# Performance work log

Measured on AMD Instinct MI355X. Metric: run time of the kernel, lower is better.

The kernel has to match this reference:

```python
import jax, jax.numpy as jnp
import numpy as np

N_CTX = 4096
D_MODEL = 1024
D_HEAD = 64


def setup_inputs() -> dict:
    key = jax.random.key(0)
    k_x, k_q, k_k, k_o, k_v = jax.random.split(key, 5)
    return {
        "x": jax.random.normal(k_x, (N_CTX, D_MODEL), dtype=jnp.float32),
        "W_q": jax.random.normal(k_q, (D_MODEL, D_HEAD), dtype=jnp.float32),
        "W_kT": jax.random.normal(k_k, (D_HEAD, D_MODEL), dtype=jnp.float32),
        "W_o": jax.random.normal(k_o, (D_MODEL, D_HEAD), dtype=jnp.float32),
        "W_vT": jax.random.normal(k_v, (D_HEAD, D_MODEL), dtype=jnp.float32),
    }


def reference(x, W_q, W_kT, W_o, W_vT):
    # x: [n, d_model]
    n = x.shape[0]
    q = x @ W_q                      # [n, d_head]
    k = x @ W_kT.T                   # [n, d_head]  (W_kT @ x.T transposed)
    scores = q @ k.T                 # [n, n] -- NOTE: original has no 1/sqrt(d_head) scaling
    # causal mask: upper triangle (strictly above diagonal) set to -inf
    causal = jnp.tril(jnp.ones((n, n), dtype=bool))
    scores = jnp.where(causal, scores, -jnp.inf)
    attn = jax.nn.softmax(scores, axis=1)  # softmax over keys (dim=1)
    v = x @ W_o @ W_vT               # [n, d_model] -- faithful to attn @ x @ W_o @ W_vT
    return attn @ v                  # [n, d_model]
```

## Files before the change

kernel.cpp:

```cpp
#include <hip/hip_runtime.h>
#include <hip/hip_bf16.h>
#include <math.h>

#define DM    1024
#define DH    64
#define NCTX  4096
#define NCH   8

typedef __attribute__((ext_vector_type(8))) short bf16x8;
typedef __attribute__((ext_vector_type(4))) float f32x4;

#define D_QH   0
#define D_QM   524288
#define D_QL   1048576
#define D_KH   1572864
#define D_KM   2097152
#define D_KL   2621440
#define D_UTB  3145728
#define D_PY   3670016
#define D_PM   12058624
#define D_PL   12189696
#define D_WTH  12320768
#define D_WTM  12713984

#define S_WVH  0
#define S_WVM  131072
#define S_PM   262144
#define S_PL   393216
#define S_PY   524288
#define S_END  8912896
#define S_YH   262144
#define S_YM   786432

__device__ __forceinline__ ushort f2bf(float x) {
  __hip_bfloat16 h = __float2bfloat16(x);
  return __builtin_bit_cast(ushort, h);
}
__device__ __forceinline__ float bf2f(ushort u) {
  __hip_bfloat16 h = __builtin_bit_cast(__hip_bfloat16, u);
  return __bfloat162float(h);
}

typedef __attribute__((address_space(1))) const unsigned int gas_u32;
typedef __attribute__((address_space(3))) unsigned int las_u32;
__device__ __forceinline__ void gload_lds16(const void* g, void* l) {
  __builtin_amdgcn_global_load_lds((gas_u32*)g, (las_u32*)l, 16, 0, 0);
}

__global__ __launch_bounds__(256) void wsplit_kernel(
    const float* __restrict__ Wq, const float* __restrict__ WkT,
    const float* __restrict__ Wo, const float* __restrict__ Wv,
    ushort* __restrict__ WTh, ushort* __restrict__ WTm,
    ushort* __restrict__ WvTh, ushort* __restrict__ WvTm)
{
  int gid = blockIdx.x * 256 + threadIdx.x;
  int mat = gid >> 16;
  int idx = gid & 65535;
  if (mat == 3) {
    float v = Wv[idx];
    int h = idx >> 10, c = idx & 1023;
    int oidx = c * 64 + h;
    ushort h16 = f2bf(v);
    WvTh[oidx] = h16;
    WvTm[oidx] = f2bf(v - bf2f(h16));
    return;
  }
  float v; int oidx;
  if (mat == 1) {
    v = WkT[idx];
    oidx = 65536 + idx;
  } else {
    int k = idx >> 6, h = idx & 63;
    v = (mat == 0 ? Wq : Wo)[idx];
    oidx = mat * 65536 + h * 1024 + k;
  }
  ushort h16 = f2bf(v);
  float rem = v - bf2f(h16);
  WTh[oidx] = h16;
  WTm[oidx] = f2bf(rem);
}

__global__ __launch_bounds__(256, 2) void proj_mfma_kernel(
    const float* __restrict__ x,
    const ushort* __restrict__ WTh, const ushort* __restrict__ WTm,
    ushort* __restrict__ Qh, ushort* __restrict__ Qm, ushort* __restrict__ Ql,
    ushort* __restrict__ Kh, ushort* __restrict__ Km, ushort* __restrict__ Kl,
    ushort* __restrict__ UTb)
{
  __shared__ __align__(16) ushort xsh[32*128], xsm[32*128];
  __shared__ __align__(16) ushort wsh[2][64*128], wsm[2][64*128];

  const int tid  = threadIdx.x;
  const int lane = tid & 63;
  const int w    = tid >> 6;
  const int q16  = lane & 15;
  const int grp  = lane >> 4;
  const int r0   = blockIdx.x * 32;
  const int mat  = blockIdx.y;
  const ushort* __restrict__ wh = WTh + mat * 65536;
  const ushort* __restrict__ wm = WTm + mat * 65536;

  const int rw  = (w & 1) * 16;
  const int ct0 = (w >> 1) * 2;

  const int xrowl = tid >> 4, xslot = tid & 15;

  auto stage_w = [&](int b, int s) {
    const int kp0 = s * 128;
    #pragma unroll
    for (int u = 0; u < 4; ++u) {
      int ubase = u * 256 + w * 64;
      int unit  = ubase + lane;
      int row   = unit >> 4, slotp = unit & 15;
      int ssrc  = slotp ^ (row & 15);
      int gsrc  = row * DM + kp0 + ssrc * 8;
      gload_lds16(&wh[gsrc], &wsh[b][ubase * 8]);
      gload_lds16(&wm[gsrc], &wsm[b][ubase * 8]);
    }
  };
  auto xload = [&](int s, float4& a0, float4& a1, float4& b0, float4& b1) {
    const int kp0 = s * 128;
    const float* s0 = &x[(r0 + xrowl) * DM + kp0 + xslot * 8];
    const float* s1 = &x[(r0 + xrowl + 16) * DM + kp0 + xslot * 8];
    a0 = *(const float4*)&s0[0]; a1 = *(const float4*)&s0[4];
    b0 = *(const float4*)&s1[0]; b1 = *(const float4*)&s1[4];
  };
  auto xsplit_write = [&](float4 a0, float4 a1, float4 b0, float4 b1) {
    float xv0[8] = {a0.x,a0.y,a0.z,a0.w,a1.x,a1.y,a1.z,a1.w};
    float xv1[8] = {b0.x,b0.y,b0.z,b0.w,b1.x,b1.y,b1.z,b1.w};
    bf16x8 hv0, mv0, hv1, mv1;
    #pragma unroll
    for (int e = 0; e < 8; ++e) {
      ushort h0 = f2bf(xv0[e]);
      hv0[e] = (short)h0;  mv0[e] = (short)f2bf(xv0[e] - bf2f(h0));
      ushort h1 = f2bf(xv1[e]);
      hv1[e] = (short)h1;  mv1[e] = (short)f2bf(xv1[e] - bf2f(h1));
    }
    int d0 = xrowl * 128 + ((xslot ^ (xrowl & 15)) << 3);
    int r1 = xrowl + 16;
    int d1 = r1 * 128 + ((xslot ^ (r1 & 15)) << 3);
    *(bf16x8*)&xsh[d0] = hv0;  *(bf16x8*)&xsm[d0] = mv0;
    *(bf16x8*)&xsh[d1] = hv1;  *(bf16x8*)&xsm[d1] = mv1;
  };

  f32x4 acc[2] = {{0,0,0,0},{0,0,0,0}};

  {
    float4 a0, a1, b0, b1;
    xload(0, a0, a1, b0, b1);
    xsplit_write(a0, a1, b0, b1);
    stage_w(0, 0);
  }
  __syncthreads();

  int cur = 0;
  for (int stg = 0; stg < 8; ++stg) {
    float4 na0, na1, nb0, nb1;
    if (stg < 7) {
      xload(stg + 1, na0, na1, nb0, nb1);
      stage_w(cur ^ 1, stg + 1);
    }
    #pragma unroll
    for (int ksub = 0; ksub < 4; ++ksub) {
      const int s = ksub * 4 + grp;
      const int xrow = rw + q16;
      bf16x8 xh8 = *(const bf16x8*)&xsh[xrow * 128 + ((s ^ (xrow & 15)) << 3)];
      bf16x8 xm8 = *(const bf16x8*)&xsm[xrow * 128 + ((s ^ (xrow & 15)) << 3)];
      #pragma unroll
      for (int i = 0; i < 2; ++i) {
        const int wrow = (ct0 + i) * 16 + q16;
        const int woff = wrow * 128 + ((s ^ (wrow & 15)) << 3);
        bf16x8 bh = *(const bf16x8*)&wsh[cur][woff];
        bf16x8 bm = *(const bf16x8*)&wsm[cur][woff];
        if (mat == 2) {
          acc[i] = __builtin_amdgcn_mfma_f32_16x16x32_bf16(bh, xh8, acc[i], 0,0,0);
          acc[i] = __builtin_amdgcn_mfma_f32_16x16x32_bf16(bh, xm8, acc[i], 0,0,0);
          acc[i] = __builtin_amdgcn_mfma_f32_16x16x32_bf16(bm, xh8, acc[i], 0,0,0);
          acc[i] = __builtin_amdgcn_mfma_f32_16x16x32_bf16(bm, xm8, acc[i], 0,0,0);
        } else {
          acc[i] = __builtin_amdgcn_mfma_f32_16x16x32_bf16(xh8, bh, acc[i], 0,0,0);
          acc[i] = __builtin_amdgcn_mfma_f32_16x16x32_bf16(xh8, bm, acc[i], 0,0,0);
          acc[i] = __builtin_amdgcn_mfma_f32_16x16x32_bf16(xm8, bh, acc[i], 0,0,0);
          acc[i] = __builtin_amdgcn_mfma_f32_16x16x32_bf16(xm8, bm, acc[i], 0,0,0);
        }
      }
    }
    __syncthreads();
    if (stg < 7) xsplit_write(na0, na1, nb0, nb1);
    __syncthreads();
    cur ^= 1;
  }

  if (mat == 2) {
    #pragma unroll
    for (int i = 0; i < 2; ++i)
      #pragma unroll
      for (int r = 0; r < 4; ++r)
        UTb[((ct0 + i)*16 + 4*grp + r) * NCTX + r0 + rw + q16] = f2bf(acc[i][r]);
  } else {
    ushort* __restrict__ Dh = (mat == 0) ? Qh : Kh;
    ushort* __restrict__ Dm = (mat == 0) ? Qm : Km;
    ushort* __restrict__ Dl = (mat == 0) ? Ql : Kl;
    #pragma unroll
    for (int i = 0; i < 2; ++i)
      #pragma unroll
      for (int r = 0; r < 4; ++r) {
        float v = acc[i][r];
        ushort h = f2bf(v); float fh = bf2f(h);
        ushort m = f2bf(v - fh); float fm = bf2f(m);
        ushort l = f2bf(v - fh - fm);
        int idx = (r0 + rw + 4*grp + r) * DH + (ct0 + i)*16 + q16;
        Dh[idx] = h; Dm[idx] = m; Dl[idx] = l;
      }
  }
}

__global__ __launch_bounds__(256, 2) void attn_kernel(
    const ushort* __restrict__ Qh, const ushort* __restrict__ Qm, const ushort* __restrict__ Ql,
    const ushort* __restrict__ Kh, const ushort* __restrict__ Km, const ushort* __restrict__ Kl,
    const ushort* __restrict__ UTb,
    float* __restrict__ Pm, float* __restrict__ Pl, float* __restrict__ Py)
{
  __shared__ ushort Ksh[2][3][64*64];
  __shared__ ushort Ush[2][64*64];
  __shared__ __align__(16) ushort ps[4][16*72];

  const int tid  = threadIdx.x;
  const int lane = tid & 63;
  const int w    = tid >> 6;
  ushort* psw = ps[w];
  const int q16  = lane & 15;
  const int grp  = lane >> 4;
  const int colb = grp * 8;

  const int qq    = blockIdx.x;
  const int c     = blockIdx.y;
  const int gbase = 252 - 4 * qq;
  const int g     = gbase + w;
  const int gmax  = gbase + 3;
  const int T     = ((16*gmax + 15) >> 6) + 1;
  const int t0 = (c * T) >> 3, t1 = ((c+1) * T) >> 3;
  const int Town = ((16*g + 15) >> 6) + 1;
  const int q0 = 16 * g;
  const int q  = q0 + q16;

  auto stage = [&](int b, int t) {
    const int j0 = t * 64;
    #pragma unroll
    for (int it = 0; it < 2; ++it) {
      int ubase = it * 256 + w * 64;
      int unit  = ubase + lane;
      int row   = unit >> 3, slotp = unit & 7;
      int c8    = slotp ^ (row & 7);
      int src   = (j0 + row) * DH + c8 * 8;
      gload_lds16(&Kh[src], &Ksh[b][0][ubase * 8]);
      gload_lds16(&Km[src], &Ksh[b][1][ubase * 8]);
      gload_lds16(&Kl[src], &Ksh[b][2][ubase * 8]);
      gload_lds16(&UTb[row * NCTX + j0 + c8 * 8], &Ush[b][ubase * 8]);
    }
  };

  bf16x8 fqh[2], fqm[2], fql[2];
  #pragma unroll
  for (int ks = 0; ks < 2; ++ks) {
    int off = (q0 + q16)*DH + 32*ks + colb;
    fqh[ks] = *(const bf16x8*)&Qh[off];
    fqm[ks] = *(const bf16x8*)&Qm[off];
    fql[ks] = *(const bf16x8*)&Ql[off];
  }

  float mrun = -3.0e38f, lrun = 0.f;
  f32x4 yacc[4] = {{0,0,0,0},{0,0,0,0},{0,0,0,0},{0,0,0,0}};

  if (t0 < t1) stage(0, t0);
  __syncthreads();

  int cur = 0;
  for (int t = t0; t < t1; ++t) {
    if (t + 1 < t1) stage(cur ^ 1, t + 1);
    if (t < Town) {
      const int j0 = t * 64;
      f32x4 sa[4] = {{0,0,0,0},{0,0,0,0},{0,0,0,0},{0,0,0,0}};
      #pragma unroll
      for (int ks = 0; ks < 2; ++ks) {
        #pragma unroll
        for (int st = 0; st < 4; ++st) {
          int row = 16*st + q16;
          int off = row * 64 + (((4*ks + grp) ^ (row & 7)) << 3);
          bf16x8 kh = *(const bf16x8*)&Ksh[cur][0][off];
          bf16x8 km = *(const bf16x8*)&Ksh[cur][1][off];
          bf16x8 kl = *(const bf16x8*)&Ksh[cur][2][off];
          sa[st] = __builtin_amdgcn_mfma_f32_16x16x32_bf16(kh, fqh[ks], sa[st], 0,0,0);
          sa[st] = __builtin_amdgcn_mfma_f32_16x16x32_bf16(kh, fqm[ks], sa[st], 0,0,0);
          sa[st] = __builtin_amdgcn_mfma_f32_16x16x32_bf16(km, fqh[ks], sa[st], 0,0,0);
          sa[st] = __builtin_amdgcn_mfma_f32_16x16x32_bf16(km, fqm[ks], sa[st], 0,0,0);
          sa[st] = __builtin_amdgcn_mfma_f32_16x16x32_bf16(kh, fql[ks], sa[st], 0,0,0);
          sa[st] = __builtin_amdgcn_mfma_f32_16x16x32_bf16(kl, fqh[ks], sa[st], 0,0,0);
        }
      }
      #pragma unroll
      for (int st = 0; st < 4; ++st)
        #pragma unroll
        for (int r = 0; r < 4; ++r) {
          int key = j0 + 16*st + 4*grp + r;
          if (key > q) sa[st][r] = -3.0e38f;
        }
      float mx = sa[0][0];
      #pragma unroll
      for (int st = 0; st < 4; ++st)
        #pragma unroll
        for (int r = 0; r < 4; ++r) mx = fmaxf(mx, sa[st][r]);
      mx = fmaxf(mx, __shfl_xor(mx, 16));
      mx = fmaxf(mx, __shfl_xor(mx, 32));
      float mnew  = fmaxf(mrun, mx);
      float alpha = __expf(mrun - mnew);
      float ts = 0.f;
      ushort pb[16];
      #pragma unroll
      for (int st = 0; st < 4; ++st)
        #pragma unroll
        for (int r = 0; r < 4; ++r) {
          float p = __expf(sa[st][r] - mnew);
          ts += p;
          pb[st*4 + r] = f2bf(p);
        }
      ts += __shfl_xor(ts, 16);
      ts += __shfl_xor(ts, 32);
      lrun = lrun * alpha + ts;
      mrun = mnew;
      float ar[4];
      #pragma unroll
      for (int r = 0; r < 4; ++r) ar[r] = __shfl(alpha, 4*grp + r, 64);
      #pragma unroll
      for (int dt = 0; dt < 4; ++dt) {
        yacc[dt][0] *= ar[0]; yacc[dt][1] *= ar[1];
        yacc[dt][2] *= ar[2]; yacc[dt][3] *= ar[3];
      }
      #pragma unroll
      for (int st = 0; st < 4; ++st) {
        uint2 v;
        v.x = (uint)pb[st*4+0] | ((uint)pb[st*4+1] << 16);
        v.y = (uint)pb[st*4+2] | ((uint)pb[st*4+3] << 16);
        *(uint2*)&psw[q16*72 + 16*st + 4*grp] = v;
      }
      __threadfence_block();
      __builtin_amdgcn_sched_barrier(0);
      #pragma unroll
      for (int ks = 0; ks < 2; ++ks) {
        bf16x8 pa = *(const bf16x8*)&psw[q16*72 + 32*ks + colb];
        #pragma unroll
        for (int dt = 0; dt < 4; ++dt) {
          int row = 16*dt + q16;
          int off = row * 64 + (((4*ks + grp) ^ (row & 7)) << 3);
          bf16x8 ub = *(const bf16x8*)&Ush[cur][off];
          yacc[dt] = __builtin_amdgcn_mfma_f32_16x16x32_bf16(pa, ub, yacc[dt], 0,0,0);
        }
      }
    }
    __syncthreads();
    cur ^= 1;
  }
  if (grp == 0) {
    Pm[c * NCTX + q] = mrun;
    Pl[c * NCTX + q] = lrun;
  }
  #pragma unroll
  for (int dt = 0; dt < 4; ++dt)
    #pragma unroll
    for (int r = 0; r < 4; ++r)
      Py[(c * NCTX + q0 + 4*grp + r) * DH + 16*dt + q16] = yacc[dt][r];
}

__global__ __launch_bounds__(256, 3) void out_fused_kernel(
    const float* __restrict__ Pm, const float* __restrict__ Pl,
    const float* __restrict__ Py,
    const ushort* __restrict__ WvTh, const ushort* __restrict__ WvTm,
    float* __restrict__ out)
{
  __shared__ __align__(16) ushort Yh[64*64], Ym[64*64];
  __shared__ __align__(16) ushort Wsh[128*64], Wsm[128*64];
  __shared__ float sden[NCH][64];
  __shared__ float invd[64];

  const int tid  = threadIdx.x;
  const int lane = tid & 63;
  const int w    = tid >> 6;
  const int q16  = lane & 15;
  const int grp  = lane >> 4;
  const int r0   = blockIdx.x * 64;
  const int cb   = blockIdx.y;

  #pragma unroll
  for (int u = 0; u < 4; ++u) {
    int ubase = u * 256 + w * 64;
    int unit  = ubase + lane;
    int row   = unit >> 3, slotp = unit & 7;
    int c8    = slotp ^ (row & 7);
    int src   = (cb * 128 + row) * 64 + c8 * 8;
    gload_lds16(&WvTh[src], &Wsh[ubase * 8]);
    gload_lds16(&WvTm[src], &Wsm[ubase * 8]);
  }
  if (tid < 64) {
    int rrow = r0 + tid;
    float mv[NCH]; float M = -3.0e38f;
    #pragma unroll
    for (int c = 0; c < NCH; ++c) {
      mv[c] = Pm[c*NCTX + rrow];
      M = fmaxf(M, mv[c]);
    }
    float den = 0.f;
    #pragma unroll
    for (int c = 0; c < NCH; ++c) {
      float s = __expf(mv[c] - M);
      sden[c][tid] = s;
      den += s * Pl[c*NCTX + rrow];
    }
    invd[tid] = 1.0f / den;
  }
  __syncthreads();

  #pragma unroll
  for (int it = 0; it < 4; ++it) {
    int idx = it * 256 + tid;
    int h4 = idx & 15, rr = idx >> 4;
    int rrow = r0 + rr;
    float nx = 0.f, ny = 0.f, nz = 0.f, nw = 0.f;
    #pragma unroll
    for (int c = 0; c < NCH; ++c) {
      float s = sden[c][rr];
      float4 p4 = *(const float4*)&Py[(c*NCTX + rrow)*DH + h4*4];
      nx += s*p4.x; ny += s*p4.y; nz += s*p4.z; nw += s*p4.w;
    }
    float inv = invd[rr];
    float yv[4] = {nx*inv, ny*inv, nz*inv, nw*inv};
    ushort hv[4], mv4[4];
    #pragma unroll
    for (int e = 0; e < 4; ++e) {
      ushort h = f2bf(yv[e]);
      hv[e] = h;
      mv4[e] = f2bf(yv[e] - bf2f(h));
    }
    int off = rr*64 + (((h4 >> 1) ^ (rr & 7)) << 3) + (h4 & 1) * 4;
    uint2 vh, vm;
    vh.x = (uint)hv[0] | ((uint)hv[1] << 16);
    vh.y = (uint)hv[2] | ((uint)hv[3] << 16);
    vm.x = (uint)mv4[0] | ((uint)mv4[1] << 16);
    vm.y = (uint)mv4[2] | ((uint)mv4[3] << 16);
    *(uint2*)&Yh[off] = vh;
    *(uint2*)&Ym[off] = vm;
  }
  __syncthreads();

  f32x4 acc[4][2] = {};
  #pragma unroll
  for (int ks = 0; ks < 2; ++ks) {
    bf16x8 ah[4], am[4];
    #pragma unroll
    for (int rt = 0; rt < 4; ++rt) {
      int row = 16*rt + q16;
      int off = row*64 + (((4*ks + grp) ^ (row & 7)) << 3);
      ah[rt] = *(const bf16x8*)&Yh[off];
      am[rt] = *(const bf16x8*)&Ym[off];
    }
    #pragma unroll
    for (int lt = 0; lt < 2; ++lt) {
      int crow = w*32 + lt*16 + q16;
      int off  = crow*64 + (((4*ks + grp) ^ (crow & 7)) << 3);
      bf16x8 bh = *(const bf16x8*)&Wsh[off];
      bf16x8 bm = *(const bf16x8*)&Wsm[off];
      #pragma unroll
      for (int rt = 0; rt < 4; ++rt) {
        acc[rt][lt] = __builtin_amdgcn_mfma_f32_16x16x32_bf16(ah[rt], bh, acc[rt][lt], 0,0,0);
        acc[rt][lt] = __builtin_amdgcn_mfma_f32_16x16x32_bf16(ah[rt], bm, acc[rt][lt], 0,0,0);
        acc[rt][lt] = __builtin_amdgcn_mfma_f32_16x16x32_bf16(am[rt], bh, acc[rt][lt], 0,0,0);
        acc[rt][lt] = __builtin_amdgcn_mfma_f32_16x16x32_bf16(am[rt], bm, acc[rt][lt], 0,0,0);
      }
    }
  }
  #pragma unroll
  for (int rt = 0; rt < 4; ++rt)
    #pragma unroll
    for (int lt = 0; lt < 2; ++lt)
      #pragma unroll
      for (int r = 0; r < 4; ++r)
        out[(r0 + 16*rt + 4*grp + r) * DM + cb*128 + w*32 + lt*16 + q16] = acc[rt][lt][r];
}

__global__ __launch_bounds__(256) void combine_kernel(
    const float* __restrict__ Pm, const float* __restrict__ Pl,
    const float* __restrict__ Py,
    ushort* __restrict__ Yh, ushort* __restrict__ Ym)
{
  int idx = blockIdx.x * 256 + threadIdx.x;
  int r = idx >> 6, d = idx & 63;
  float mv[NCH];
  float M = -3.0e38f;
  #pragma unroll
  for (int c = 0; c < NCH; ++c) {
    mv[c] = Pm[c*NCTX + r];
    M = fmaxf(M, mv[c]);
  }
  float num = 0.f, den = 0.f;
  #pragma unroll
  for (int c = 0; c < NCH; ++c) {
    float s = __expf(mv[c] - M);
    den += s * Pl[c*NCTX + r];
    num += s * Py[(c*NCTX + r)*DH + d];
  }
  float y = num / den;
  ushort h = f2bf(y);
  Yh[idx] = h;
  Ym[idx] = f2bf(y - bf2f(h));
}

__global__ __launch_bounds__(256, 3) void out_mfma_kernel(
    const ushort* __restrict__ Yh_g, const ushort* __restrict__ Ym_g,
    const ushort* __restrict__ WvTh, const ushort* __restrict__ WvTm,
    float* __restrict__ out)
{
  __shared__ __align__(16) ushort Yh[64*64], Ym[64*64];
  __shared__ __align__(16) ushort Wsh[128*64], Wsm[128*64];

  const int tid  = threadIdx.x;
  const int lane = tid & 63;
  const int w    = tid >> 6;
  const int q16  = lane & 15;
  const int grp  = lane >> 4;
  const int r0   = blockIdx.x * 64;
  const int cb   = blockIdx.y;

  #pragma unroll
  for (int it = 0; it < 2; ++it) {
    int ubase = it * 256 + w * 64;
    int unit  = ubase + lane;
    int row   = unit >> 3, slotp = unit & 7;
    int c8    = slotp ^ (row & 7);
    int src   = (r0 + row) * 64 + c8 * 8;
    gload_lds16(&Yh_g[src], &Yh[ubase * 8]);
    gload_lds16(&Ym_g[src], &Ym[ubase * 8]);
  }
  #pragma unroll
  for (int u = 0; u < 4; ++u) {
    int ubase = u * 256 + w * 64;
    int unit  = ubase + lane;
    int row   = unit >> 3, slotp = unit & 7;
    int c8    = slotp ^ (row & 7);
    int src   = (cb * 128 + row) * 64 + c8 * 8;
    gload_lds16(&WvTh[src], &Wsh[ubase * 8]);
    gload_lds16(&WvTm[src], &Wsm[ubase * 8]);
  }
  __syncthreads();

  f32x4 acc[4][2] = {};
  #pragma unroll
  for (int ks = 0; ks < 2; ++ks) {
    bf16x8 ah[4], am[4];
    #pragma unroll
    for (int rt = 0; rt < 4; ++rt) {
      int row = 16*rt + q16;
      int off = row*64 + (((4*ks + grp) ^ (row & 7)) << 3);
      ah[rt] = *(const bf16x8*)&Yh[off];
      am[rt] = *(const bf16x8*)&Ym[off];
    }
    #pragma unroll
    for (int lt = 0; lt < 2; ++lt) {
      int crow = w*32 + lt*16 + q16;
      int off  = crow*64 + (((4*ks + grp) ^ (crow & 7)) << 3);
      bf16x8 bh = *(const bf16x8*)&Wsh[off];
      bf16x8 bm = *(const bf16x8*)&Wsm[off];
      #pragma unroll
      for (int rt = 0; rt < 4; ++rt) {
        acc[rt][lt] = __builtin_amdgcn_mfma_f32_16x16x32_bf16(ah[rt], bh, acc[rt][lt], 0,0,0);
        acc[rt][lt] = __builtin_amdgcn_mfma_f32_16x16x32_bf16(ah[rt], bm, acc[rt][lt], 0,0,0);
        acc[rt][lt] = __builtin_amdgcn_mfma_f32_16x16x32_bf16(am[rt], bh, acc[rt][lt], 0,0,0);
        acc[rt][lt] = __builtin_amdgcn_mfma_f32_16x16x32_bf16(am[rt], bm, acc[rt][lt], 0,0,0);
      }
    }
  }
  #pragma unroll
  for (int rt = 0; rt < 4; ++rt)
    #pragma unroll
    for (int lt = 0; lt < 2; ++lt)
      #pragma unroll
      for (int r = 0; r < 4; ++r)
        out[(r0 + 16*rt + 4*grp + r) * DM + cb*128 + w*32 + lt*16 + q16] = acc[rt][lt][r];
}

extern "C" void kernel_launch(void* const* d_in, const int* in_sizes, int n_in,
                              void* d_out, int out_size, void* d_ws, size_t ws_size,
                              hipStream_t stream) {
  const float* x   = (const float*)d_in[0];
  const float* Wq  = (const float*)d_in[1];
  const float* WkT = (const float*)d_in[2];
  const float* Wo  = (const float*)d_in[3];
  const float* Wv  = (const float*)d_in[4];
  float* out = (float*)d_out;
  char*  ob  = (char*)d_out;
  char*  wb  = (char*)d_ws;

  ushort* Qhp = (ushort*)(ob + D_QH);
  ushort* Qmp = (ushort*)(ob + D_QM);
  ushort* Qlp = (ushort*)(ob + D_QL);
  ushort* Khp = (ushort*)(ob + D_KH);
  ushort* Kmp = (ushort*)(ob + D_KM);
  ushort* Klp = (ushort*)(ob + D_KL);
  ushort* UTb = (ushort*)(ob + D_UTB);
  ushort* WTh = (ushort*)(ob + D_WTH);
  ushort* WTm = (ushort*)(ob + D_WTM);

  ushort* WvTh = (ushort*)(wb + S_WVH);
  ushort* WvTm = (ushort*)(wb + S_WVM);

  const bool big_ws = (ws_size >= (size_t)S_END);

  float* Pmp = big_ws ? (float*)(wb + S_PM) : (float*)(ob + D_PM);
  float* Plp = big_ws ? (float*)(wb + S_PL) : (float*)(ob + D_PL);
  float* Pyp = big_ws ? (float*)(wb + S_PY) : (float*)(ob + D_PY);

  hipLaunchKernelGGL(wsplit_kernel, dim3(1024), dim3(256), 0, stream,
                     Wq, WkT, Wo, Wv, WTh, WTm, WvTh, WvTm);
  hipLaunchKernelGGL(proj_mfma_kernel, dim3(128, 3), dim3(256), 0, stream,
                     x, WTh, WTm, Qhp, Qmp, Qlp, Khp, Kmp, Klp, UTb);
  hipLaunchKernelGGL(attn_kernel, dim3(64, 8), dim3(256), 0, stream,
                     Qhp, Qmp, Qlp, Khp, Kmp, Klp, UTb, Pmp, Plp, Pyp);
  if (big_ws) {
    hipLaunchKernelGGL(out_fused_kernel, dim3(64, 8), dim3(256), 0, stream,
                       Pmp, Plp, Pyp, WvTh, WvTm, out);
  } else {
    ushort* Yhp = (ushort*)(wb + S_YH);
    ushort* Ymp = (ushort*)(wb + S_YM);
    hipLaunchKernelGGL(combine_kernel, dim3(1024), dim3(256), 0, stream,
                       Pmp, Plp, Pyp, Yhp, Ymp);
    hipLaunchKernelGGL(out_mfma_kernel, dim3(64, 8), dim3(256), 0, stream,
                       Yhp, Ymp, WvTh, WvTm, out);
  }
}
```

Baseline: 58.48 us.

## Switch split-precision MFMA from bf16 to fp16 and drop low-order terms

Result: faster. 55.08 us (median of 2 runs) (-5.8%).

```diff
diff --git a/kernel.cpp b/kernel.cpp
--- a/kernel.cpp
+++ b/kernel.cpp
@@ -7,15 +7,13 @@
 #define NCTX  4096
 #define NCH   8
 
-typedef __attribute__((ext_vector_type(8))) short bf16x8;
+typedef __attribute__((ext_vector_type(8))) _Float16 f16x8;
 typedef __attribute__((ext_vector_type(4))) float f32x4;
 
 #define D_QH   0
 #define D_QM   524288
-#define D_QL   1048576
 #define D_KH   1572864
 #define D_KM   2097152
-#define D_KL   2621440
 #define D_UTB  3145728
 #define D_PY   3670016
 #define D_PM   12058624
@@ -32,13 +30,12 @@
 #define S_YH   262144
 #define S_YM   786432
 
-__device__ __forceinline__ ushort f2bf(float x) {
-  __hip_bfloat16 h = __float2bfloat16(x);
+__device__ __forceinline__ ushort f2h(float x) {
+  _Float16 h = (_Float16)x;
   return __builtin_bit_cast(ushort, h);
 }
-__device__ __forceinline__ float bf2f(ushort u) {
-  __hip_bfloat16 h = __builtin_bit_cast(__hip_bfloat16, u);
-  return __bfloat162float(h);
+__device__ __forceinline__ float h2f(ushort u) {
+  return (float)__builtin_bit_cast(_Float16, u);
 }
 
 typedef __attribute__((address_space(1))) const unsigned int gas_u32;
@@ -60,9 +57,9 @@
     float v = Wv[idx];
     int h = idx >> 10, c = idx & 1023;
     int oidx = c * 64 + h;
-    ushort h16 = f2bf(v);
+    ushort h16 = f2h(v);
     WvTh[oidx] = h16;
-    WvTm[oidx] = f2bf(v - bf2f(h16));
+    WvTm[oidx] = f2h(v - h2f(h16));
     return;
   }
   float v; int oidx;
@@ -74,17 +71,17 @@
     v = (mat == 0 ? Wq : Wo)[idx];
     oidx = mat * 65536 + h * 1024 + k;
   }
-  ushort h16 = f2bf(v);
-  float rem = v - bf2f(h16);
+  ushort h16 = f2h(v);
+  float rem = v - h2f(h16);
   WTh[oidx] = h16;
-  WTm[oidx] = f2bf(rem);
+  WTm[oidx] = f2h(rem);
 }
 
 __global__ __launch_bounds__(256, 2) void proj_mfma_kernel(
     const float* __restrict__ x,
     const ushort* __restrict__ WTh, const ushort* __restrict__ WTm,
-    ushort* __restrict__ Qh, ushort* __restrict__ Qm, ushort* __restrict__ Ql,
-    ushort* __restrict__ Kh, ushort* __restrict__ Km, ushort* __restrict__ Kl,
+    ushort* __restrict__ Qh, ushort* __restrict__ Qm,
+    ushort* __restrict__ Kh, ushort* __restrict__ Km,
     ushort* __restrict__ UTb)
 {
   __shared__ __align__(16) ushort xsh[32*128], xsm[32*128];
@@ -128,19 +125,22 @@
   auto xsplit_write = [&](float4 a0, float4 a1, float4 b0, float4 b1) {
     float xv0[8] = {a0.x,a0.y,a0.z,a0.w,a1.x,a1.y,a1.z,a1.w};
     float xv1[8] = {b0.x,b0.y,b0.z,b0.w,b1.x,b1.y,b1.z,b1.w};
-    bf16x8 hv0, mv0, hv1, mv1;
+    ushort hv0[8], mv0[8], hv1[8], mv1[8];
     #pragma unroll
     for (int e = 0; e < 8; ++e) {
-      ushort h0 = f2bf(xv0[e]);
-      hv0[e] = (short)h0;  mv0[e] = (short)f2bf(xv0[e] - bf2f(h0));
-      ushort h1 = f2bf(xv1[e]);
-      hv1[e] = (short)h1;  mv1[e] = (short)f2bf(xv1[e] - bf2f(h1));
+      ushort h0 = f2h(xv0[e]);
+      hv0[e] = h0;  mv0[e] = f2h(xv0[e] - h2f(h0));
+      ushort h1 = f2h(xv1[e]);
+      hv1[e] = h1;  mv1[e] = f2h(xv1[e] - h2f(h1));
     }
     int d0 = xrowl * 128 + ((xslot ^ (xrowl & 15)) << 3);
     int r1 = xrowl + 16;
     int d1 = r1 * 128 + ((xslot ^ (r1 & 15)) << 3);
-    *(bf16x8*)&xsh[d0] = hv0;  *(bf16x8*)&xsm[d0] = mv0;
-    *(bf16x8*)&xsh[d1] = hv1;  *(bf16x8*)&xsm[d1] = mv1;
+    #pragma unroll
+    for (int e = 0; e < 8; ++e) {
+      xsh[d0+e] = hv0[e]; xsm[d0+e] = mv0[e];
+      xsh[d1+e] = hv1[e]; xsm[d1+e] = mv1[e];
+    }
   };
 
   f32x4 acc[2] = {{0,0,0,0},{0,0,0,0}};
@@ -164,24 +164,22 @@
     for (int ksub = 0; ksub < 4; ++ksub) {
       const int s = ksub * 4 + grp;
       const int xrow = rw + q16;
-      bf16x8 xh8 = *(const bf16x8*)&xsh[xrow * 128 + ((s ^ (xrow & 15)) << 3)];
-      bf16x8 xm8 = *(const bf16x8*)&xsm[xrow * 128 + ((s ^ (xrow & 15)) << 3)];
+      f16x8 xh8 = *(const f16x8*)&xsh[xrow * 128 + ((s ^ (xrow & 15)) << 3)];
+      f16x8 xm8 = *(const f16x8*)&xsm[xrow * 128 + ((s ^ (xrow & 15)) << 3)];
       #pragma unroll
       for (int i = 0; i < 2; ++i) {
         const int wrow = (ct0 + i) * 16 + q16;
         const int woff = wrow * 128 + ((s ^ (wrow & 15)) << 3);
-        bf16x8 bh = *(const bf16x8*)&wsh[cur][woff];
-        bf16x8 bm = *(const bf16x8*)&wsm[cur][woff];
+        f16x8 bh = *(const f16x8*)&wsh[cur][woff];
+        f16x8 bm = *(const f16x8*)&wsm[cur][woff];
         if (mat == 2) {
-          acc[i] = __builtin_amdgcn_mfma_f32_16x16x32_bf16(bh, xh8, acc[i], 0,0,0);
-          acc[i] = __builtin_amdgcn_mfma_f32_16x16x32_bf16(bh, xm8, acc[i], 0,0,0);
-          acc[i] = __builtin_amdgcn_mfma_f32_16x16x32_bf16(bm, xh8, acc[i], 0,0,0);
-          acc[i] = __builtin_amdgcn_mfma_f32_16x16x32_bf16(bm, xm8, acc[i], 0,0,0);
+          acc[i] = __builtin_amdgcn_mfma_f32_16x16x32_f16(bh, xh8, acc[i], 0,0,0);
+          acc[i] = __builtin_amdgcn_mfma_f32_16x16x32_f16(bh, xm8, acc[i], 0,0,0);
+          acc[i] = __builtin_amdgcn_mfma_f32_16x16x32_f16(bm, xh8, acc[i], 0,0,0);
         } else {
-          acc[i] = __builtin_amdgcn_mfma_f32_16x16x32_bf16(xh8, bh, acc[i], 0,0,0);
-          acc[i] = __builtin_amdgcn_mfma_f32_16x16x32_bf16(xh8, bm, acc[i], 0,0,0);
-          acc[i] = __builtin_amdgcn_mfma_f32_16x16x32_bf16(xm8, bh, acc[i], 0,0,0);
-          acc[i] = __builtin_amdgcn_mfma_f32_16x16x32_bf16(xm8, bm, acc[i], 0,0,0);
+          acc[i] = __builtin_amdgcn_mfma_f32_16x16x32_f16(xh8, bh, acc[i], 0,0,0);
+          acc[i] = __builtin_amdgcn_mfma_f32_16x16x32_f16(xh8, bm, acc[i], 0,0,0);
+          acc[i] = __builtin_amdgcn_mfma_f32_16x16x32_f16(xm8, bh, acc[i], 0,0,0);
         }
       }
     }
@@ -196,32 +194,30 @@
     for (int i = 0; i < 2; ++i)
       #pragma unroll
       for (int r = 0; r < 4; ++r)
-        UTb[((ct0 + i)*16 + 4*grp + r) * NCTX + r0 + rw + q16] = f2bf(acc[i][r]);
+        UTb[((ct0 + i)*16 + 4*grp + r) * NCTX + r0 + rw + q16] = f2h(acc[i][r]);
   } else {
     ushort* __restrict__ Dh = (mat == 0) ? Qh : Kh;
     ushort* __restrict__ Dm = (mat == 0) ? Qm : Km;
-    ushort* __restrict__ Dl = (mat == 0) ? Ql : Kl;
     #pragma unroll
     for (int i = 0; i < 2; ++i)
       #pragma unroll
       for (int r = 0; r < 4; ++r) {
         float v = acc[i][r];
-        ushort h = f2bf(v); float fh = bf2f(h);
-        ushort m = f2bf(v - fh); float fm = bf2f(m);
-        ushort l = f2bf(v - fh - fm);
+        ushort h = f2h(v);
+        ushort m = f2h(v - h2f(h));
         int idx = (r0 + rw + 4*grp + r) * DH + (ct0 + i)*16 + q16;
-        Dh[idx] = h; Dm[idx] = m; Dl[idx] = l;
+        Dh[idx] = h; Dm[idx] = m;
       }
   }
 }
 
 __global__ __launch_bounds__(256, 2) void attn_kernel(
-    const ushort* __restrict__ Qh, const ushort* __restrict__ Qm, const ushort* __restrict__ Ql,
-    const ushort* __restrict__ Kh, const ushort* __restrict__ Km, const ushort* __restrict__ Kl,
+    const ushort* __restrict__ Qh, const ushort* __restrict__ Qm,
+    const ushort* __restrict__ Kh, const ushort* __restrict__ Km,
     const ushort* __restrict__ UTb,
     float* __restrict__ Pm, float* __restrict__ Pl, float* __restrict__ Py)
 {
-  __shared__ ushort Ksh[2][3][64*64];
+  __shared__ ushort Ksh[2][2][64*64];
   __shared__ ushort Ush[2][64*64];
   __shared__ __align__(16) ushort ps[4][16*72];
 
@@ -255,18 +251,16 @@
       int src   = (j0 + row) * DH + c8 * 8;
       gload_lds16(&Kh[src], &Ksh[b][0][ubase * 8]);
       gload_lds16(&Km[src], &Ksh[b][1][ubase * 8]);
-      gload_lds16(&Kl[src], &Ksh[b][2][ubase * 8]);
       gload_lds16(&UTb[row * NCTX + j0 + c8 * 8], &Ush[b][ubase * 8]);
     }
   };
 
-  bf16x8 fqh[2], fqm[2], fql[2];
+  f16x8 fqh[2], fqm[2];
   #pragma unroll
   for (int ks = 0; ks < 2; ++ks) {
     int off = (q0 + q16)*DH + 32*ks + colb;
-    fqh[ks] = *(const bf16x8*)&Qh[off];
-    fqm[ks] = *(const bf16x8*)&Qm[off];
-    fql[ks] = *(const bf16x8*)&Ql[off];
+    fqh[ks] = *(const f16x8*)&Qh[off];
+    fqm[ks] = *(const f16x8*)&Qm[off];
   }
 
   float mrun = -3.0e38f, lrun = 0.f;
@@ -287,15 +281,11 @@
         for (int st = 0; st < 4; ++st) {
           int row = 16*st + q16;
           int off = row * 64 + (((4*ks + grp) ^ (row & 7)) << 3);
-          bf16x8 kh = *(const bf16x8*)&Ksh[cur][0][off];
-          bf16x8 km = *(const bf16x8*)&Ksh[cur][1][off];
-          bf16x8 kl = *(const bf16x8*)&Ksh[cur][2][off];
-          sa[st] = __builtin_amdgcn_mfma_f32_16x16x32_bf16(kh, fqh[ks], sa[st], 0,0,0);
-          sa[st] = __builtin_amdgcn_mfma_f32_16x16x32_bf16(kh, fqm[ks], sa[st], 0,0,0);
-          sa[st] = __builtin_amdgcn_mfma_f32_16x16x32_bf16(km, fqh[ks], sa[st], 0,0,0);
-          sa[st] = __builtin_amdgcn_mfma_f32_16x16x32_bf16(km, fqm[ks], sa[st], 0,0,0);
-          sa[st] = __builtin_amdgcn_mfma_f32_16x16x32_bf16(kh, fql[ks], sa[st], 0,0,0);
-          sa[st] = __builtin_amdgcn_mfma_f32_16x16x32_bf16(kl, fqh[ks], sa[st], 0,0,0);
+          f16x8 kh = *(const f16x8*)&Ksh[cur][0][off];
+          f16x8 km = *(const f16x8*)&Ksh[cur][1][off];
+          sa[st] = __builtin_amdgcn_mfma_f32_16x16x32_f16(kh, fqh[ks], sa[st], 0,0,0);
+          sa[st] = __builtin_amdgcn_mfma_f32_16x16x32_f16(kh, fqm[ks], sa[st], 0,0,0);
+          sa[st] = __builtin_amdgcn_mfma_f32_16x16x32_f16(km, fqh[ks], sa[st], 0,0,0);
         }
       }
       #pragma unroll
@@ -322,7 +312,7 @@
         for (int r = 0; r < 4; ++r) {
           float p = __expf(sa[st][r] - mnew);
           ts += p;
-          pb[st*4 + r] = f2bf(p);
+          pb[st*4 + r] = f2h(p);
         }
       ts += __shfl_xor(ts, 16);
       ts += __shfl_xor(ts, 32);
@@ -347,13 +337,13 @@
       __builtin_amdgcn_sched_barrier(0);
       #pragma unroll
       for (int ks = 0; ks < 2; ++ks) {
-        bf16x8 pa = *(const bf16x8*)&psw[q16*72 + 32*ks + colb];
+        f16x8 pa = *(const f16x8*)&psw[q16*72 + 32*ks + colb];
         #pragma unroll
         for (int dt = 0; dt < 4; ++dt) {
           int row = 16*dt + q16;
           int off = row * 64 + (((4*ks + grp) ^ (row & 7)) << 3);
-          bf16x8 ub = *(const bf16x8*)&Ush[cur][off];
-          yacc[dt] = __builtin_amdgcn_mfma_f32_16x16x32_bf16(pa, ub, yacc[dt], 0,0,0);
+          f16x8 ub = *(const f16x8*)&Ush[cur][off];
+          yacc[dt] = __builtin_amdgcn_mfma_f32_16x16x32_f16(pa, ub, yacc[dt], 0,0,0);
         }
       }
     }
@@ -436,9 +426,9 @@
     ushort hv[4], mv4[4];
     #pragma unroll
     for (int e = 0; e < 4; ++e) {
-      ushort h = f2bf(yv[e]);
+      ushort h = f2h(yv[e]);
       hv[e] = h;
-      mv4[e] = f2bf(yv[e] - bf2f(h));
+      mv4[e] = f2h(yv[e] - h2f(h));
     }
     int off = rr*64 + (((h4 >> 1) ^ (rr & 7)) << 3) + (h4 & 1) * 4;
     uint2 vh, vm;
@@ -454,26 +444,25 @@
   f32x4 acc[4][2] = {};
   #pragma unroll
   for (int ks = 0; ks < 2; ++ks) {
-    bf16x8 ah[4], am[4];
+    f16x8 ah[4], am[4];
     #pragma unroll
     for (int rt = 0; rt < 4; ++rt) {
       int row = 16*rt + q16;
       int off = row*64 + (((4*ks + grp) ^ (row & 7)) << 3);
-      ah[rt] = *(const bf16x8*)&Yh[off];
-      am[rt] = *(const bf16x8*)&Ym[off];
+      ah[rt] = *(const f16x8*)&Yh[off];
+      am[rt] = *(const f16x8*)&Ym[off];
     }
     #pragma unroll
     for (int lt = 0; lt < 2; ++lt) {
       int crow = w*32 + lt*16 + q16;
       int off  = crow*64 + (((4*ks + grp) ^ (crow & 7)) << 3);
-      bf16x8 bh = *(const bf16x8*)&Wsh[off];
-      bf16x8 bm = *(const bf16x8*)&Wsm[off];
+      f16x8 bh = *(const f16x8*)&Wsh[off];
+      f16x8 bm = *(const f16x8*)&Wsm[off];
       #pragma unroll
       for (int rt = 0; rt < 4; ++rt) {
-        acc[rt][lt] = __builtin_amdgcn_mfma_f32_16x16x32_bf16(ah[rt], bh, acc[rt][lt], 0,0,0);
-        acc[rt][lt] = __builtin_amdgcn_mfma_f32_16x16x32_bf16(ah[rt], bm, acc[rt][lt], 0,0,0);
-        acc[rt][lt] = __builtin_amdgcn_mfma_f32_16x16x32_bf16(am[rt], bh, acc[rt][lt], 0,0,0);
-        acc[rt][lt] = __builtin_amdgcn_mfma_f32_16x16x32_bf16(am[rt], bm, acc[rt][lt], 0,0,0);
+        acc[rt][lt] = __builtin_amdgcn_mfma_f32_16x16x32_f16(ah[rt], bh, acc[rt][lt], 0,0,0);
+        acc[rt][lt] = __builtin_amdgcn_mfma_f32_16x16x32_f16(ah[rt], bm, acc[rt][lt], 0,0,0);
+        acc[rt][lt] = __builtin_amdgcn_mfma_f32_16x16x32_f16(am[rt], bh, acc[rt][lt], 0,0,0);
       }
     }
   }
@@ -508,9 +497,9 @@
     num += s * Py[(c*NCTX + r)*DH + d];
   }
   float y = num / den;
-  ushort h = f2bf(y);
+  ushort h = f2h(y);
   Yh[idx] = h;
-  Ym[idx] = f2bf(y - bf2f(h));
+  Ym[idx] = f2h(y - h2f(h));
 }
 
 __global__ __launch_bounds__(256, 3) void out_mfma_kernel(
@@ -554,26 +543,25 @@
   f32x4 acc[4][2] = {};
   #pragma unroll
   for (int ks = 0; ks < 2; ++ks) {
-    bf16x8 ah[4], am[4];
+    f16x8 ah[4], am[4];
     #pragma unroll
     for (int rt = 0; rt < 4; ++rt) {
       int row = 16*rt + q16;
       int off = row*64 + (((4*ks + grp) ^ (row & 7)) << 3);
-      ah[rt] = *(const bf16x8*)&Yh[off];
-      am[rt] = *(const bf16x8*)&Ym[off];
+      ah[rt] = *(const f16x8*)&Yh[off];
+      am[rt] = *(const f16x8*)&Ym[off];
     }
     #pragma unroll
     for (int lt = 0; lt < 2; ++lt) {
       int crow = w*32 + lt*16 + q16;
       int off  = crow*64 + (((4*ks + grp) ^ (crow & 7)) << 3);
-      bf16x8 bh = *(const bf16x8*)&Wsh[off];
-      bf16x8 bm = *(const bf16x8*)&Wsm[off];
+      f16x8 bh = *(const f16x8*)&Wsh[off];
+      f16x8 bm = *(const f16x8*)&Wsm[off];
       #pragma unroll
       for (int rt = 0; rt < 4; ++rt) {
-        acc[rt][lt] = __builtin_amdgcn_mfma_f32_16x16x32_bf16(ah[rt], bh, acc[rt][lt], 0,0,0);
-        acc[rt][lt] = __builtin_amdgcn_mfma_f32_16x16x32_bf16(ah[rt], bm, acc[rt][lt], 0,0,0);
-        acc[rt][lt] = __builtin_amdgcn_mfma_f32_16x16x32_bf16(am[rt], bh, acc[rt][lt], 0,0,0);
-        acc[rt][lt] = __builtin_amdgcn_mfma_f32_16x16x32_bf16(am[rt], bm, acc[rt][lt], 0,0,0);
+        acc[rt][lt] = __builtin_amdgcn_mfma_f32_16x16x32_f16(ah[rt], bh, acc[rt][lt], 0,0,0);
+        acc[rt][lt] = __builtin_amdgcn_mfma_f32_16x16x32_f16(ah[rt], bm, acc[rt][lt], 0,0,0);
+        acc[rt][lt] = __builtin_amdgcn_mfma_f32_16x16x32_f16(am[rt], bh, acc[rt][lt], 0,0,0);
       }
     }
   }
@@ -600,10 +588,8 @@
 
   ushort* Qhp = (ushort*)(ob + D_QH);
   ushort* Qmp = (ushort*)(ob + D_QM);
-  ushort* Qlp = (ushort*)(ob + D_QL);
   ushort* Khp = (ushort*)(ob + D_KH);
   ushort* Kmp = (ushort*)(ob + D_KM);
-  ushort* Klp = (ushort*)(ob + D_KL);
   ushort* UTb = (ushort*)(ob + D_UTB);
   ushort* WTh = (ushort*)(ob + D_WTH);
   ushort* WTm = (ushort*)(ob + D_WTM);
@@ -620,9 +606,9 @@
   hipLaunchKernelGGL(wsplit_kernel, dim3(1024), dim3(256), 0, stream,
                      Wq, WkT, Wo, Wv, WTh, WTm, WvTh, WvTm);
   hipLaunchKernelGGL(proj_mfma_kernel, dim3(128, 3), dim3(256), 0, stream,
-                     x, WTh, WTm, Qhp, Qmp, Qlp, Khp, Kmp, Klp, UTb);
+                     x, WTh, WTm, Qhp, Qmp, Khp, Kmp, UTb);
   hipLaunchKernelGGL(attn_kernel, dim3(64, 8), dim3(256), 0, stream,
-                     Qhp, Qmp, Qlp, Khp, Kmp, Klp, UTb, Pmp, Plp, Pyp);
+                     Qhp, Qmp, Khp, Kmp, UTb, Pmp, Plp, Pyp);
   if (big_ws) {
     hipLaunchKernelGGL(out_fused_kernel, dim3(64, 8), dim3(256), 0, stream,
                        Pmp, Plp, Pyp, WvTh, WvTm, out);
```
